# Performance work log

Measured on AMD Instinct MI355X. Metric: run time of the kernel, lower is better.

## Reference

```python
import jax, jax.numpy as jnp
import numpy as np

N_EMBD = 1024
N_HEAD = 16
B, T = 2, 2048

def setup_inputs() -> dict:
    key = jax.random.key(0)
    ks = jax.random.split(key, 5)
    s = 1.0 / np.sqrt(N_EMBD)
    return {
        'x': jax.random.normal(ks[0], (B, T, N_EMBD), jnp.float32),
        'W_attn': jax.random.normal(ks[1], (N_EMBD, 3 * N_EMBD), jnp.float32) * s,
        'b_attn': jax.random.normal(ks[2], (3 * N_EMBD,), jnp.float32) * 0.02,
        'W_proj': jax.random.normal(ks[3], (N_EMBD, N_EMBD), jnp.float32) * s,
        'b_proj': jax.random.normal(ks[4], (N_EMBD,), jnp.float32) * 0.02,
    }

def reference(x, W_attn, b_attn, W_proj, b_proj):
    Bx, Tx, C = x.shape
    H = N_HEAD
    D = C // H  # head dim
    qkv = x @ W_attn + b_attn                      # [B,T,3C]
    q, k, v = jnp.split(qkv, 3, axis=-1)
    # [B,T,C] -> [B,H,T,D]
    q = q.reshape(Bx, Tx, H, D).transpose(0, 2, 1, 3)
    k = k.reshape(Bx, Tx, H, D).transpose(0, 2, 1, 3)
    v = v.reshape(Bx, Tx, H, D).transpose(0, 2, 1, 3)
    scale = 1.0 / jnp.sqrt(jnp.asarray(D, x.dtype))
    scores = jnp.einsum('bhqd,bhkd->bhqk', q, k) * scale   # [B,H,T,T]
    causal = jnp.tril(jnp.ones((Tx, Tx), bool))
    scores = jnp.where(causal, scores, jnp.asarray(-jnp.inf, scores.dtype))
    attn = jax.nn.softmax(scores, axis=-1)
    y = jnp.einsum('bhqk,bhkd->bhqd', attn, v)              # [B,H,T,D]
    y = y.transpose(0, 2, 1, 3).reshape(Bx, Tx, C)
    return y @ W_proj + b_proj
```

## Files before the change

### kernel.cpp

```cpp
#include <hip/hip_runtime.h>
#include <stdint.h>

typedef float f32x4 __attribute__((ext_vector_type(4)));
typedef float f32x16 __attribute__((ext_vector_type(16)));
typedef __bf16 bf16x8 __attribute__((ext_vector_type(8)));
typedef unsigned short ushort8 __attribute__((ext_vector_type(8)));
typedef unsigned int uint4v __attribute__((ext_vector_type(4)));
typedef unsigned short u16;

#define DEVINL static __device__ __forceinline__

#define EXP2(x) exp2f(x)

#define VMCNT(N)                                          \
  {                                                       \
    asm volatile("s_waitcnt vmcnt(" #N ")" ::: "memory"); \
    __builtin_amdgcn_sched_barrier(0);                    \
  }

DEVINL void barrier_raw() {
  __builtin_amdgcn_sched_barrier(0);
  __builtin_amdgcn_s_barrier();
  __builtin_amdgcn_sched_barrier(0);
}

DEVINL u16 f2bf(float f) {
  __bf16 h = (__bf16)f;
  return __builtin_bit_cast(u16, h);
}

DEVINL unsigned cvtpk(float lo, float hi) {
  unsigned r;
  asm("v_cvt_pk_bf16_f32 %0, %1, %2" : "=v"(r) : "v"(lo), "v"(hi));
  return r;
}

DEVINL void plswap(unsigned& a, unsigned& b) {
  asm("v_permlane32_swap_b32 %0, %1" : "+v"(a), "+v"(b));
}

DEVINL void gload16(const void* g, void* l) {
  __builtin_amdgcn_global_load_lds((__attribute__((address_space(1))) void*)g,
                                   (__attribute__((address_space(3))) void*)l, 16, 0, 0);
}

DEVINL f32x4 mfma16(bf16x8 a, bf16x8 b, f32x4 c) {
  return __builtin_amdgcn_mfma_f32_16x16x32_bf16(a, b, c, 0, 0, 0);
}
DEVINL f32x16 mfma32(bf16x8 a, bf16x8 b, f32x16 c) {
  return __builtin_amdgcn_mfma_f32_32x32x16_bf16(a, b, c, 0, 0, 0);
}

__global__ __launch_bounds__(256) void k_prep(const float* __restrict__ x,
                                              u16* __restrict__ xb,
                                              const float* __restrict__ Wa,
                                              u16* __restrict__ WaT,
                                              const float* __restrict__ Wp,
                                              u16* __restrict__ WpT) {
  __shared__ float tile[32][33];
  const int bid = blockIdx.x;
  if (bid < 2048) {
    const int i = bid * 256 + threadIdx.x;
    const float4* p = (const float4*)x + (size_t)i * 2;
    float4 a = p[0], b = p[1];
    ushort8 o;
    o[0] = f2bf(a.x); o[1] = f2bf(a.y); o[2] = f2bf(a.z); o[3] = f2bf(a.w);
    o[4] = f2bf(b.x); o[5] = f2bf(b.y); o[6] = f2bf(b.z); o[7] = f2bf(b.w);
    *((ushort8*)xb + i) = o;
    return;
  }
  const float* in;
  u16* out;
  int C, cx, ry;
  if (bid < 5120) {
    const int bx = bid - 2048;
    in = Wa; out = WaT; C = 3072; cx = bx % 96; ry = bx / 96;
  } else {
    const int bx = bid - 5120;
    in = Wp; out = WpT; C = 1024; cx = bx & 31; ry = bx >> 5;
  }
  const int tx = threadIdx.x & 31, ty = threadIdx.x >> 5;
  const int c0 = cx * 32, r0 = ry * 32;
#pragma unroll
  for (int k = 0; k < 4; ++k)
    tile[ty + k * 8][tx] = in[(size_t)(r0 + ty + k * 8) * C + (c0 + tx)];
  __syncthreads();
#pragma unroll
  for (int k = 0; k < 4; ++k)
    out[(size_t)(c0 + ty + k * 8) * 1024 + (r0 + tx)] = f2bf(tile[tx][ty + k * 8]);
}

template <int ROWS>
DEVINL void stageRx64(const u16* __restrict__ g, int ld, u16* lds, int t) {
#pragma unroll
  for (int i = 0; i < ROWS / 32; ++i) {
    int ci = i * 256 + t;
    int row = ci >> 3, gr = ci & 7;
    int gs = gr ^ (row & 7);
    gload16(g + (size_t)row * ld + gs * 8, lds + ci * 8);
  }
}

template <int ROWS>
DEVINL void stageRx32(const u16* __restrict__ g, int ld, u16* lds, int t) {
#pragma unroll
  for (int i = 0; i < ROWS / 64; ++i) {
    int ci = i * 256 + t;
    int row = ci >> 2, gr = ci & 3;
    int gs = gr ^ ((row >> 1) & 3);
    gload16(g + (size_t)row * ld + gs * 8, lds + ci * 8);
  }
}

DEVINL void gemm_core_128b32(const u16* __restrict__ A, const u16* __restrict__ B,
                             int Kdim, u16* As, u16* Bs, int t, f32x4 acc[4][4]) {
  const int l = t & 63, lr = l & 15, lg = l >> 4;
  const int wr = t >> 7, wc = (t >> 6) & 1;
  const int nk = Kdim >> 5;
  stageRx32<128>(A, Kdim, As, t);
  stageRx32<128>(B, Kdim, Bs, t);
  for (int kt = 0; kt < nk; ++kt) {
    if (kt + 1 < nk) {
      stageRx32<128>(A + (kt + 1) * 32, Kdim, As + ((kt + 1) & 1) * 4096, t);
      stageRx32<128>(B + (kt + 1) * 32, Kdim, Bs + ((kt + 1) & 1) * 4096, t);
      VMCNT(4);
    } else {
      VMCNT(0);
    }
    barrier_raw();
    const u16* Asc = As + (kt & 1) * 4096;
    const u16* Bsc = Bs + (kt & 1) * 4096;
    bf16x8 af[4], bf[4];
#pragma unroll
    for (int mi = 0; mi < 4; ++mi) {
      int r = wr * 64 + mi * 16 + lr;
      int g = lg ^ ((r >> 1) & 3);
      af[mi] = *(const bf16x8*)(Asc + r * 32 + g * 8);
    }
#pragma unroll
    for (int ni = 0; ni < 4; ++ni) {
      int r = wc * 64 + ni * 16 + lr;
      int g = lg ^ ((r >> 1) & 3);
      bf[ni] = *(const bf16x8*)(Bsc + r * 32 + g * 8);
    }
#pragma unroll
    for (int mi = 0; mi < 4; ++mi)
#pragma unroll
      for (int ni = 0; ni < 4; ++ni)
        acc[mi][ni] = mfma16(af[mi], bf[ni], acc[mi][ni]);
    barrier_raw();
  }
}

DEVINL void gemm_core_64(const u16* __restrict__ A, const u16* __restrict__ B,
                         int Kdim, u16* As, u16* Bs, int t, f32x4 acc[2][4]) {
  const int l = t & 63, lr = l & 15, lg = l >> 4;
  const int wr = t >> 7, wc = (t >> 6) & 1;
  const int nk = Kdim >> 6;
  stageRx64<64>(A, Kdim, As, t);
  stageRx64<128>(B, Kdim, Bs, t);
  for (int kt = 0; kt < nk; ++kt) {
    if (kt + 1 < nk) {
      stageRx64<64>(A + (kt + 1) * 64, Kdim, As + ((kt + 1) & 1) * 4096, t);
      stageRx64<128>(B + (kt + 1) * 64, Kdim, Bs + ((kt + 1) & 1) * 8192, t);
      VMCNT(6);
    } else {
      VMCNT(0);
    }
    barrier_raw();
    const u16* Asc = As + (kt & 1) * 4096;
    const u16* Bsc = Bs + (kt & 1) * 8192;
#pragma unroll
    for (int ks = 0; ks < 2; ++ks) {
      bf16x8 af[2], bf[4];
#pragma unroll
      for (int mi = 0; mi < 2; ++mi) {
        int r = wr * 32 + mi * 16 + lr;
        int g = (ks * 4 + lg) ^ (r & 7);
        af[mi] = *(const bf16x8*)(Asc + r * 64 + g * 8);
      }
#pragma unroll
      for (int ni = 0; ni < 4; ++ni) {
        int r = wc * 64 + ni * 16 + lr;
        int g = (ks * 4 + lg) ^ (r & 7);
        bf[ni] = *(const bf16x8*)(Bsc + r * 64 + g * 8);
      }
#pragma unroll
      for (int mi = 0; mi < 2; ++mi)
#pragma unroll
        for (int ni = 0; ni < 4; ++ni)
          acc[mi][ni] = mfma16(af[mi], bf[ni], acc[mi][ni]);
    }
    barrier_raw();
  }
}

__global__ __launch_bounds__(256) void k_gemm_qkv(const u16* __restrict__ xb,
                                                  const u16* __restrict__ WaT,
                                                  const float* __restrict__ b_attn,
                                                  u16* __restrict__ Qo,
                                                  u16* __restrict__ Ko,
                                                  u16* __restrict__ Vto) {
  __shared__ u16 As[2 * 128 * 32], Bs[2 * 128 * 32];
  const int t = threadIdx.x;
  const int m0 = blockIdx.y * 128, n0 = blockIdx.x * 128;
  f32x4 acc[4][4] = {};
  gemm_core_128b32(xb + (size_t)m0 * 1024, WaT + (size_t)n0 * 1024, 1024, As, Bs, t,
                   acc);
  const int l = t & 63, lr = l & 15, lg = l >> 4;
  const int wr = t >> 7, wc = (t >> 6) & 1;
#pragma unroll
  for (int ni = 0; ni < 4; ++ni) {
    const int gcol = n0 + wc * 64 + ni * 16 + lr;
    const int part = gcol >> 10;
    const int h = (gcol & 1023) >> 6, d = gcol & 63;
    const float bias = b_attn[gcol];
    if (part == 2) {
#pragma unroll
      for (int mi = 0; mi < 4; ++mi) {
        const int tt0 = m0 + wr * 64 + mi * 16 + lg * 4;
        const int bb = tt0 >> 11, tt = tt0 & 2047;
        ushort4 pk;
        pk.x = f2bf(acc[mi][ni][0] + bias);
        pk.y = f2bf(acc[mi][ni][1] + bias);
        pk.z = f2bf(acc[mi][ni][2] + bias);
        pk.w = f2bf(acc[mi][ni][3] + bias);
        *(ushort4*)(Vto + (size_t)(bb * 16 + h) * 131072 + (size_t)d * 2048 + tt) = pk;
      }
    } else {
      const float osc = (part == 0) ? 0.18033688f : 1.0f;
      u16* dst = (part == 0) ? Qo : Ko;
#pragma unroll
      for (int mi = 0; mi < 4; ++mi)
#pragma unroll
        for (int r = 0; r < 4; ++r) {
          const int grow = m0 + wr * 64 + mi * 16 + lg * 4 + r;
          const int bb = grow >> 11, tt = grow & 2047;
          dst[(size_t)((bb * 16 + h) * 2048 + tt) * 64 + d] =
              f2bf((acc[mi][ni][r] + bias) * osc);
        }
    }
  }
}

__global__ __launch_bounds__(256) void k_gemm_proj(const u16* __restrict__ Yb,
                                                   const u16* __restrict__ WpT,
                                                   const float* __restrict__ b_proj,
                                                   float* __restrict__ out) {
  __shared__ u16 As[2 * 64 * 64], Bs[2 * 128 * 64];
  const int t = threadIdx.x;
  const int m0 = blockIdx.y * 64, n0 = blockIdx.x * 128;
  f32x4 acc[2][4] = {};
  gemm_core_64(Yb + (size_t)m0 * 1024, WpT + (size_t)n0 * 1024, 1024, As, Bs, t, acc);
  const int l = t & 63, lr = l & 15, lg = l >> 4;
  const int wr = t >> 7, wc = (t >> 6) & 1;
#pragma unroll
  for (int ni = 0; ni < 4; ++ni) {
    const int gcol = n0 + wc * 64 + ni * 16 + lr;
    const float bias = b_proj[gcol];
#pragma unroll
    for (int mi = 0; mi < 2; ++mi)
#pragma unroll
      for (int r = 0; r < 4; ++r) {
        const int grow = m0 + wr * 32 + mi * 16 + lg * 4 + r;
        out[(size_t)grow * 1024 + gcol] = acc[mi][ni][r] + bias;
      }
  }
}

__global__ __launch_bounds__(1024, 4) void k_flash(const u16* __restrict__ Q,
                                                   const u16* __restrict__ K,
                                                   const u16* __restrict__ Vt,
                                                   u16* __restrict__ Y) {
  __shared__ u16 SM[2 * 9216 + 2 * 8704];
  u16* KsB = SM;
  u16* VsB = SM + 2 * 9216;
  float* Ms = (float*)SM;

  const int t = threadIdx.x, l = t & 63, w = t >> 6;
  const int ql = l & 31, hi = l >> 5;
  const int wq = w & 3, wk = w >> 2;
  const int bid = blockIdx.x;
  const int bh = (bid & 7) + 8 * ((bid >> 3) & 3);
  const int p = bid >> 5;
  const size_t base = (size_t)bh * 131072;
  const int b = bh >> 4, hh = bh & 15;
  const int srow = t >> 3, scol = t & 7;
  const int sd = t >> 4, sck = t & 15;

  for (int half = 0; half < 2; ++half) {
    const int qt = half ? 15 - p : p;
    const int nsteps = qt + 1;
    const int qbase = qt * 128 + wq * 32;
    const int qrow = qbase + ql;

    __syncthreads();

    bf16x8 qb[4];
#pragma unroll
    for (int m = 0; m < 4; ++m)
      qb[m] = *(const bf16x8*)(Q + base + (size_t)qrow * 64 + hi * 8 + 16 * m);

    {
      ushort8 kv = *(const ushort8*)(K + base + (size_t)srow * 64 + scol * 8);
      ushort8 vv = *(const ushort8*)(Vt + base + (size_t)sd * 2048 + sck * 8);
      *(ushort8*)(KsB + srow * 72 + scol * 8) = kv;
      *(ushort8*)(VsB + sd * 136 + sck * 8) = vv;
    }
    __syncthreads();

    f32x16 accO0 = {}, accO1 = {};
    float rs_lane = 0.f;
    const int krow = wk * 32 + ql;

    for (int n = 0; n < nsteps; ++n) {
      const u16* Kc = KsB + (n & 1) * 9216;
      const u16* Vc = VsB + (n & 1) * 8704;
      const bool more = (n + 1 < nsteps);
      ushort8 kv, vv;
      if (more) {
        kv = *(const ushort8*)(K + base + (size_t)((n + 1) * 128 + srow) * 64 + scol * 8);
        vv = *(const ushort8*)(Vt + base + (size_t)sd * 2048 + (n + 1) * 128 + sck * 8);
      }
      const int kbase = n * 128 + wk * 32;
      if (kbase <= qbase + 31) {
        f32x16 st = {};
        __builtin_amdgcn_s_setprio(1);
#pragma unroll
        for (int m = 0; m < 4; ++m) {
          bf16x8 ka = *(const bf16x8*)(Kc + krow * 72 + (hi + 2 * m) * 8);
          st = mfma32(ka, qb[m], st);
        }
        __builtin_amdgcn_s_setprio(0);
        if (kbase + 31 > qbase) {
#pragma unroll
          for (int r = 0; r < 16; ++r) {
            const int keyl = (r & 3) + 8 * (r >> 2) + 4 * hi;
            if (kbase + keyl > qrow) st[r] = -1e30f;
          }
        }
        float pp[16];
#pragma unroll
        for (int r = 0; r < 16; ++r) {
          pp[r] = EXP2(st[r]);
          rs_lane += pp[r];
        }
        unsigned uu[8];
#pragma unroll
        for (int i = 0; i < 8; ++i) uu[i] = cvtpk(pp[2 * i], pp[2 * i + 1]);
        plswap(uu[0], uu[2]);
        plswap(uu[1], uu[3]);
        plswap(uu[4], uu[6]);
        plswap(uu[5], uu[7]);
        uint4v w0 = {uu[0], uu[1], uu[2], uu[3]};
        uint4v w1 = {uu[4], uu[5], uu[6], uu[7]};
        bf16x8 pf0 = __builtin_bit_cast(bf16x8, w0);
        bf16x8 pf1 = __builtin_bit_cast(bf16x8, w1);
        __builtin_amdgcn_s_setprio(1);
        {
          bf16x8 va0 = *(const bf16x8*)(Vc + ql * 136 + (4 * wk + hi) * 8);
          bf16x8 va1 = *(const bf16x8*)(Vc + ql * 136 + (4 * wk + 2 + hi) * 8);
          accO0 = mfma32(va0, pf0, accO0);
          accO0 = mfma32(va1, pf1, accO0);
          bf16x8 vb0 = *(const bf16x8*)(Vc + (32 + ql) * 136 + (4 * wk + hi) * 8);
          bf16x8 vb1 = *(const bf16x8*)(Vc + (32 + ql) * 136 + (4 * wk + 2 + hi) * 8);
          accO1 = mfma32(vb0, pf0, accO1);
          accO1 = mfma32(vb1, pf1, accO1);
        }
        __builtin_amdgcn_s_setprio(0);
      }
      if (more) {
        u16* Kn = KsB + ((n + 1) & 1) * 9216;
        u16* Vn = VsB + ((n + 1) & 1) * 8704;
        *(ushort8*)(Kn + srow * 72 + scol * 8) = kv;
        *(ushort8*)(Vn + sd * 136 + sck * 8) = vv;
      }
      __syncthreads();
    }

    rs_lane += __shfl_xor(rs_lane, 32);

    {
      float* Mp = Ms + (size_t)(((wq * 2 + (wk >> 1)) * 64 + l)) * 33;
      if (wk & 1) {
#pragma unroll
        for (int i = 0; i < 16; ++i) Mp[i] = accO0[i];
#pragma unroll
        for (int i = 0; i < 16; ++i) Mp[16 + i] = accO1[i];
        Mp[32] = rs_lane;
      }
      __syncthreads();
      if (!(wk & 1)) {
#pragma unroll
        for (int i = 0; i < 16; ++i) accO0[i] += Mp[i];
#pragma unroll
        for (int i = 0; i < 16; ++i) accO1[i] += Mp[16 + i];
        rs_lane += Mp[32];
      }
      __syncthreads();
    }
    {
      float* Mp = Ms + (size_t)((wq * 64 + l)) * 33;
      if (wk == 2) {
#pragma unroll
        for (int i = 0; i < 16; ++i) Mp[i] = accO0[i];
#pragma unroll
        for (int i = 0; i < 16; ++i) Mp[16 + i] = accO1[i];
        Mp[32] = rs_lane;
      }
      __syncthreads();
      if (wk == 0) {
        const float inv = 1.0f / (rs_lane + Mp[32]);
        u16* yb = Y + ((size_t)(b * 2048 + qrow)) * 1024 + hh * 64;
#pragma unroll
        for (int rq = 0; rq < 4; ++rq) {
          const int d0 = 8 * rq + 4 * hi;
          ushort4 o4;
          o4.x = f2bf((accO0[rq * 4 + 0] + Mp[rq * 4 + 0]) * inv);
          o4.y = f2bf((accO0[rq * 4 + 1] + Mp[rq * 4 + 1]) * inv);
          o4.z = f2bf((accO0[rq * 4 + 2] + Mp[rq * 4 + 2]) * inv);
          o4.w = f2bf((accO0[rq * 4 + 3] + Mp[rq * 4 + 3]) * inv);
          *(ushort4*)(yb + d0) = o4;
        }
#pragma unroll
        for (int rq = 0; rq < 4; ++rq) {
          const int d0 = 32 + 8 * rq + 4 * hi;
          ushort4 o4;
          o4.x = f2bf((accO1[rq * 4 + 0] + Mp[16 + rq * 4 + 0]) * inv);
          o4.y = f2bf((accO1[rq * 4 + 1] + Mp[16 + rq * 4 + 1]) * inv);
          o4.z = f2bf((accO1[rq * 4 + 2] + Mp[16 + rq * 4 + 2]) * inv);
          o4.w = f2bf((accO1[rq * 4 + 3] + Mp[16 + rq * 4 + 3]) * inv);
          *(ushort4*)(yb + d0) = o4;
        }
      }
    }
  }
}

extern "C" void kernel_launch(void* const* d_in, const int* in_sizes, int n_in,
                              void* d_out, int out_size, void* d_ws, size_t ws_size,
                              hipStream_t stream) {
  const float* x      = (const float*)d_in[0];
  const float* W_attn = (const float*)d_in[1];
  const float* b_attn = (const float*)d_in[2];
  const float* W_proj = (const float*)d_in[3];
  const float* b_proj = (const float*)d_in[4];
  float* out = (float*)d_out;

  char* ws = (char*)d_ws;
  u16* xb  = (u16*)(ws);
  u16* WaT = (u16*)(ws + (8u  << 20));
  u16* WpT = (u16*)(ws + (14u << 20));
  u16* Qb  = (u16*)(ws + (16u << 20));
  u16* Kb  = (u16*)(ws + (24u << 20));
  u16* Vtb = (u16*)(ws + (32u << 20));
  u16* Yb  = (u16*)(ws + (40u << 20));

  k_prep<<<dim3(6144), dim3(256), 0, stream>>>(x, xb, W_attn, WaT, W_proj, WpT);
  k_gemm_qkv<<<dim3(24, 32), dim3(256), 0, stream>>>(xb, WaT, b_attn, Qb, Kb, Vtb);
  k_flash<<<dim3(256), dim3(1024), 0, stream>>>(Qb, Kb, Vtb, Yb);
  k_gemm_proj<<<dim3(8, 64), dim3(256), 0, stream>>>(Yb, WpT, b_proj, out);
}
```

Before: 101.4 us.

## Triple-buffer K/V tiles in flash attention with two-step global prefetch

Switches the flash-attention kernel from double to triple LDS buffering. K/V global loads are now issued two iterations ahead and held in registers while the previous tile is written into a third buffer, giving more time to hide global latency. The __syncthreads calls are replaced by an explicit lgkmcnt(0) wait plus a raw barrier. The launch-bounds minimum blocks per CU drops from 4 to 1. The extra buffer raises LDS use and the prefetch adds register pressure, which could lower occupancy.

```diff
diff --git a/kernel.cpp b/kernel.cpp
--- a/kernel.cpp
+++ b/kernel.cpp
@@ -16,6 +16,12 @@
   {                                                       \
     asm volatile("s_waitcnt vmcnt(" #N ")" ::: "memory"); \
     __builtin_amdgcn_sched_barrier(0);                    \
+  }
+
+#define LGKM0()                                            \
+  {                                                        \
+    asm volatile("s_waitcnt lgkmcnt(0)" ::: "memory");     \
+    __builtin_amdgcn_sched_barrier(0);                     \
   }
 
 DEVINL void barrier_raw() {
@@ -268,13 +274,17 @@
   }
 }
 
-__global__ __launch_bounds__(1024, 4) void k_flash(const u16* __restrict__ Q,
+__global__ __launch_bounds__(1024, 1) void k_flash(const u16* __restrict__ Q,
                                                    const u16* __restrict__ K,
                                                    const u16* __restrict__ Vt,
                                                    u16* __restrict__ Y) {
-  __shared__ u16 SM[2 * 9216 + 2 * 8704];
-  u16* KsB = SM;
-  u16* VsB = SM + 2 * 9216;
+  __shared__ u16 SM[3 * 9216 + 3 * 8704];
+  u16* KB0 = SM;
+  u16* KB1 = SM + 9216;
+  u16* KB2 = SM + 2 * 9216;
+  u16* VB0 = SM + 3 * 9216;
+  u16* VB1 = VB0 + 8704;
+  u16* VB2 = VB0 + 2 * 8704;
   float* Ms = (float*)SM;
 
   const int t = threadIdx.x, l = t & 63, w = t >> 6;
@@ -301,26 +311,32 @@
     for (int m = 0; m < 4; ++m)
       qb[m] = *(const bf16x8*)(Q + base + (size_t)qrow * 64 + hi * 8 + 16 * m);
 
-    {
-      ushort8 kv = *(const ushort8*)(K + base + (size_t)srow * 64 + scol * 8);
-      ushort8 vv = *(const ushort8*)(Vt + base + (size_t)sd * 2048 + sck * 8);
-      *(ushort8*)(KsB + srow * 72 + scol * 8) = kv;
-      *(ushort8*)(VsB + sd * 136 + sck * 8) = vv;
-    }
-    __syncthreads();
+    ushort8 kvC, vvC;
+    kvC = *(const ushort8*)(K + base + (size_t)srow * 64 + scol * 8);
+    vvC = *(const ushort8*)(Vt + base + (size_t)sd * 2048 + sck * 8);
+    *(ushort8*)(KB0 + srow * 72 + scol * 8) = kvC;
+    *(ushort8*)(VB0 + sd * 136 + sck * 8) = vvC;
+    if (nsteps > 1) {
+      kvC = *(const ushort8*)(K + base + (size_t)(128 + srow) * 64 + scol * 8);
+      vvC = *(const ushort8*)(Vt + base + (size_t)sd * 2048 + 128 + sck * 8);
+    }
+    LGKM0();
+    barrier_raw();
+
+    u16 *Kc = KB0, *Kw = KB1, *Ksp = KB2;
+    u16 *Vc = VB0, *Vw = VB1, *Vsp = VB2;
 
     f32x16 accO0 = {}, accO1 = {};
     float rs_lane = 0.f;
     const int krow = wk * 32 + ql;
 
     for (int n = 0; n < nsteps; ++n) {
-      const u16* Kc = KsB + (n & 1) * 9216;
-      const u16* Vc = VsB + (n & 1) * 8704;
-      const bool more = (n + 1 < nsteps);
-      ushort8 kv, vv;
-      if (more) {
-        kv = *(const ushort8*)(K + base + (size_t)((n + 1) * 128 + srow) * 64 + scol * 8);
-        vv = *(const ushort8*)(Vt + base + (size_t)sd * 2048 + (n + 1) * 128 + sck * 8);
+      ushort8 kvN, vvN;
+      if (n + 2 < nsteps) {
+        kvN = *(const ushort8*)(K + base + (size_t)((n + 2) * 128 + srow) * 64 +
+                                scol * 8);
+        vvN = *(const ushort8*)(Vt + base + (size_t)sd * 2048 + (n + 2) * 128 +
+                                sck * 8);
       }
       const int kbase = n * 128 + wk * 32;
       if (kbase <= qbase + 31) {
@@ -369,13 +385,16 @@
         }
         __builtin_amdgcn_s_setprio(0);
       }
-      if (more) {
-        u16* Kn = KsB + ((n + 1) & 1) * 9216;
-        u16* Vn = VsB + ((n + 1) & 1) * 8704;
-        *(ushort8*)(Kn + srow * 72 + scol * 8) = kv;
-        *(ushort8*)(Vn + sd * 136 + sck * 8) = vv;
-      }
-      __syncthreads();
+      if (n + 1 < nsteps) {
+        *(ushort8*)(Kw + srow * 72 + scol * 8) = kvC;
+        *(ushort8*)(Vw + sd * 136 + sck * 8) = vvC;
+      }
+      LGKM0();
+      barrier_raw();
+      u16* tk = Kc; Kc = Kw; Kw = Ksp; Ksp = tk;
+      u16* tv = Vc; Vc = Vw; Vw = Vsp; Vsp = tv;
+      kvC = kvN;
+      vvC = vvN;
     }
 
     rs_lane += __shfl_xor(rs_lane, 32);
```

Result: no change. 102.5 us (+1.1%).
